# Kernel optimization log

Hardware: AMD Instinct MI355X
Metric: run time of the kernel (lower is better)

## Reference

```python
import jax, jax.numpy as jnp
import numpy as np
from jax import lax

C = 64
KS = 3  # filter_ks for dynamic kernel conv


def conv2d(x, w, pad, b=None):
    out = lax.conv_general_dilated(x, w, (1, 1), [(pad, pad), (pad, pad)],
                                   dimension_numbers=("NCHW", "OIHW", "NCHW"))
    if b is not None:
        out = out + b.reshape(1, -1, 1, 1)
    return out


def kernel_conv2d(feat, kernel):
    # feat: [B,C,H,W]; kernel: [B,C*KS*KS,H,W] -> per-pixel per-channel 3x3 filter
    B, Cc, H, W = feat.shape
    pad = (KS - 1) // 2
    xp = jnp.pad(feat, ((0, 0), (0, 0), (pad, pad), (pad, pad)), mode="edge")
    # patches: [B,C,KS*KS,H,W]
    patches = jnp.stack([xp[:, :, i:i + H, j:j + W]
                         for i in range(KS) for j in range(KS)], axis=2)
    K = kernel.reshape(B, Cc, KS * KS, H, W)
    return jnp.sum(patches * K, axis=2)


def setup_inputs() -> dict:
    key = jax.random.key(0)
    ks = jax.random.split(key, 24)
    B, H, W = 8, 128, 128
    s = lambda *sh: 1.0 / np.sqrt(np.prod(sh[1:]))
    def w(k, *sh):
        return jax.random.normal(k, sh, dtype=jnp.float32) * s(*sh)
    return {
        "f_event": jax.random.normal(ks[0], (B, C, H, W), dtype=jnp.float32),
        "f_blur": jax.random.normal(ks[1], (B, C, H, W), dtype=jnp.float32),
        # trans: conv3x3 -> ReLU -> conv3x3 (no bias)
        "Wt1": w(ks[2], C, C, 3, 3), "Wt2": w(ks[3], C, C, 3, 3),
        # trans2: conv3x3 -> ReLU
        "Wt3": w(ks[4], C, C, 3, 3),
        # F_mlp: Linear(C,2C) -> ReLU -> Linear(2C,C) -> Sigmoid
        "A1": w(ks[5], 2 * C, C), "b1": jnp.zeros((2 * C,), jnp.float32),
        "A2": w(ks[6], C, 2 * C), "b2": jnp.zeros((C,), jnp.float32),
        # gernerate_kernel: conv3x3(bias) -> ReLU -> conv1x1(bias) to C*KS^2
        "G1": w(ks[7], C, C, 3, 3), "g1b": jnp.zeros((C,), jnp.float32),
        "G2": w(ks[8], C * KS * KS, C, 1, 1), "g2b": jnp.zeros((C * KS * KS,), jnp.float32),
        # gate_rgb: conv1x1 C->1, bias
        "Rw": w(ks[9], 1, C, 1, 1), "rb": jnp.zeros((1,), jnp.float32),
        # body_sa: conv3x3 -> ReLU -> conv3x3 (no bias)
        "S1": w(ks[10], C, C, 3, 3), "S2": w(ks[11], C, C, 3, 3),
        # spatial_e: BasicConv(2,1,5,pad=2,relu=False), bias
        "Ew": w(ks[12], 1, 2, 5, 5), "eb": jnp.zeros((1,), jnp.float32),
        # conv1x1_fusion: 2C->2C, no bias
        "Fw": w(ks[13], 2 * C, 2 * C, 1, 1),
    }


def reference(f_event, f_blur, Wt1, Wt2, Wt3, A1, b1, A2, b2,
              G1, g1b, G2, g2b, Rw, rb, S1, S2, Ew, eb, Fw):
    fused = f_event + f_blur
    fused = conv2d(jax.nn.relu(conv2d(fused, Wt1, 1)), Wt2, 1)  # trans
    # SE-style channel gate
    w0 = jnp.mean(fused, axis=(2, 3))                      # [B,C]
    w0 = jax.nn.relu(w0 @ A1.T + b1)
    w0 = jax.nn.sigmoid(w0 @ A2.T + b2)                    # [B,C]
    f_b = f_blur + w0[:, :, None, None] * f_blur
    fused2 = fused + jax.nn.relu(conv2d(fused, Wt3, 1))    # trans2 + residual
    rgb_att = conv2d(fused2, Rw, 0, rb)                    # [B,1,H,W]
    f_b = f_b + rgb_att * f_b
    # dynamic per-pixel kernel from events
    kern = conv2d(jax.nn.relu(conv2d(f_event, G1, 1, g1b)), G2, 0, g2b)
    f_b = f_b + kernel_conv2d(f_b, kern)
    # spatial attention on events
    sa = conv2d(jax.nn.relu(conv2d(f_event, S1, 1)), S2, 1)
    comp = jnp.concatenate([jnp.max(sa, axis=1, keepdims=True),
                            jnp.mean(sa, axis=1, keepdims=True)], axis=1)
    scale_e = jax.nn.sigmoid(conv2d(comp, Ew, 2, eb))      # [B,1,H,W]
    f_e = f_event + scale_e * f_event
    res = conv2d(jnp.concatenate([f_e, f_b], axis=1), Fw, 0)
    return res
```

## Files before the change

kernel.cpp:

```cpp
#include <hip/hip_runtime.h>
#include <math.h>

constexpr int Bn = 8, Cn = 64, Hn = 128, Wn = 128;
constexpr int HW  = Hn * Wn;
constexpr int CHW = Cn * HW;
constexpr size_t NB = (size_t)Bn * CHW;

typedef float  f32x4  __attribute__((ext_vector_type(4)));
typedef __bf16 bf16x8 __attribute__((ext_vector_type(8)));
typedef unsigned int u32x4 __attribute__((ext_vector_type(4)));
typedef unsigned int u32x2 __attribute__((ext_vector_type(2)));

static __device__ __forceinline__ unsigned short f2bf(float f) {
    unsigned u = __builtin_bit_cast(unsigned, f);
    u = (u + 0x7FFF + ((u >> 16) & 1)) >> 16;
    return (unsigned short)u;
}
static __device__ __forceinline__ float bf2f(unsigned short v) {
    unsigned u = (unsigned)v << 16;
    return __builtin_bit_cast(float, u);
}
static __device__ __forceinline__ float bfhalf(unsigned u, int hi) {
    unsigned r = hi ? (u & 0xffff0000u) : (u << 16);
    return __builtin_bit_cast(float, r);
}

__global__ void prep_w_k(const float* __restrict__ W0, const float* __restrict__ W1,
                         const float* __restrict__ W2, const float* __restrict__ W3,
                         const float* __restrict__ W4, const float* __restrict__ W5,
                         unsigned short* __restrict__ dst) {
    int i = blockIdx.x * 256 + threadIdx.x;
    if (i >= 36864) return;
    const float* W = W0;
    switch (blockIdx.y) {
        case 1: W = W1; break; case 2: W = W2; break;
        case 3: W = W3; break; case 4: W = W4; break; case 5: W = W5; break;
        default: break;
    }
    int cj = i & 7;
    int rest = i >> 3;
    int co = rest & 63;
    rest >>= 6;
    int t  = rest % 9;
    int hs = rest / 9;
    int ci = hs * 8 + cj;
    dst[(size_t)blockIdx.y * 36864 + i] = f2bf(W[(co * 64 + ci) * 9 + t]);
}

__global__ void prep2_k(const float* __restrict__ G2, const float* __restrict__ Fw,
                        unsigned short* __restrict__ G2p, unsigned short* __restrict__ Fwp) {
    int i = blockIdx.x * 256 + threadIdx.x;
    if (i < 36864) G2p[i] = f2bf(G2[i]);
    else if (i < 36864 + 16384) Fwp[i - 36864] = f2bf(Fw[i - 36864]);
}

__global__ void pre_blk_k(const float* __restrict__ fe, const float* __restrict__ fb,
                          unsigned short* __restrict__ evb, unsigned short* __restrict__ f0b,
                          unsigned short* __restrict__ fbb) {
    int i = blockIdx.x * 256 + threadIdx.x;
    int px = i & 16383;
    int oct = (i >> 14) & 7;
    int b = i >> 17;
    const float* pe = fe + (size_t)b * CHW + (size_t)oct * 8 * HW + px;
    const float* pb = fb + (size_t)b * CHW + (size_t)oct * 8 * HW + px;
    u32x4 ev, f0, fbv;
#pragma unroll
    for (int q = 0; q < 4; ++q) {
        float e0 = pe[(size_t)(2 * q) * HW],     b0 = pb[(size_t)(2 * q) * HW];
        float e1 = pe[(size_t)(2 * q + 1) * HW], b1 = pb[(size_t)(2 * q + 1) * HW];
        ev[q]  = (unsigned)f2bf(e0) | ((unsigned)f2bf(e1) << 16);
        f0[q]  = (unsigned)f2bf(e0 + b0) | ((unsigned)f2bf(e1 + b1) << 16);
        fbv[q] = (unsigned)f2bf(b0) | ((unsigned)f2bf(b1) << 16);
    }
    const size_t o = ((size_t)(b * 8 + oct) * HW + px) * 8;
    *(u32x4*)(evb + o) = ev;
    *(u32x4*)(f0b + o) = f0;
    *(u32x4*)(fbb + o) = fbv;
}

template<bool RELU, bool BIAS, bool ADD_INPUT, bool RGB, bool COMP, bool STORE>
__global__ __launch_bounds__(256, 3) void conv3x3_blk(
        const unsigned short* __restrict__ in, const unsigned short* __restrict__ Wg,
        const float* __restrict__ bias, unsigned short* __restrict__ out,
        const float* __restrict__ gw, const float* __restrict__ gb,
        float* __restrict__ gout) {
    __shared__ unsigned short smIn[20736];
    const int b  = blockIdx.z;
    const int by = blockIdx.y << 4, bx = blockIdx.x << 4;
    const int tid = threadIdx.x;
    const int lane = tid & 63, w = tid >> 6;
    const int lx = lane & 15, ls = lane >> 4;

    for (int idx = tid; idx < 2592; idx += 256) {
        int oct = idx / 324;
        int p   = idx - oct * 324;
        int yy = p / 18, xx = p - yy * 18;
        int gy = by + yy - 1, gx = bx + xx - 1;
        u32x4 v = u32x4{0u, 0u, 0u, 0u};
        if ((unsigned)gy < (unsigned)Hn && (unsigned)gx < (unsigned)Wn)
            v = *(const u32x4*)(in + ((size_t)(b * 8 + oct) * HW + gy * Wn + gx) * 8);
        *(u32x4*)(smIn + idx * 8) = v;
    }
    __syncthreads();

    f32x4 acc[4][4];
#pragma unroll
    for (int m = 0; m < 4; ++m)
#pragma unroll
        for (int n = 0; n < 4; ++n) acc[m][n] = f32x4{0.f, 0.f, 0.f, 0.f};

#pragma unroll
    for (int ky = 0; ky < 3; ++ky)
#pragma unroll
    for (int kx = 0; kx < 3; ++kx) {
        const int t = ky * 3 + kx;
#pragma unroll
        for (int kk = 0; kk < 2; ++kk) {
            bf16x8 a[4];
            const unsigned short* wbase = Wg + kk * 18432 + ls * 4608 + t * 512 + lx * 8;
#pragma unroll
            for (int m = 0; m < 4; ++m)
                a[m] = *(const bf16x8*)(wbase + m * 128);
            const unsigned short* ibase =
                smIn + ((kk * 4 + ls) * 324 + (4 * w + ky) * 18 + lx + kx) * 8;
#pragma unroll
            for (int n = 0; n < 4; ++n) {
                bf16x8 bf = *(const bf16x8*)(ibase + n * 144);
#pragma unroll
                for (int m = 0; m < 4; ++m)
                    acc[m][n] = __builtin_amdgcn_mfma_f32_16x16x32_bf16(
                        a[m], bf, acc[m][n], 0, 0, 0);
            }
        }
    }

    const int y0 = by + 4 * w;
    float gs[4], gm[4];
    if constexpr (RGB || COMP) {
#pragma unroll
        for (int n = 0; n < 4; ++n) { gs[n] = 0.f; gm[n] = -1e30f; }
    }
#pragma unroll
    for (int m = 0; m < 4; ++m) {
        float4 rw4;
        if constexpr (RGB) rw4 = *(const float4*)(gw + 16 * m + ls * 4);
        const float rwf[4] = {RGB ? rw4.x : 0.f, RGB ? rw4.y : 0.f,
                              RGB ? rw4.z : 0.f, RGB ? rw4.w : 0.f};
        float bv[4] = {0.f, 0.f, 0.f, 0.f};
        if constexpr (BIAS) {
            float4 b4 = *(const float4*)(bias + 16 * m + ls * 4);
            bv[0] = b4.x; bv[1] = b4.y; bv[2] = b4.z; bv[3] = b4.w;
        }
        const size_t rowb = (size_t)(b * 8 + m * 2 + (ls >> 1)) * HW;
        const int j0 = (ls & 1) * 4;
#pragma unroll
        for (int n = 0; n < 4; ++n) {
            const size_t pofs = rowb + (size_t)(y0 + n) * Wn + bx + lx;
            u32x2 rin;
            if constexpr (ADD_INPUT) rin = *(const u32x2*)(in + pofs * 8 + j0);
            float vr[4];
#pragma unroll
            for (int r = 0; r < 4; ++r) {
                float v = acc[m][n][r] + bv[r];
                if constexpr (RELU) v = fmaxf(v, 0.f);
                if constexpr (ADD_INPUT) v += bfhalf(rin[r >> 1], r & 1);
                vr[r] = v;
                if constexpr (RGB) gs[n] = fmaf(rwf[r], v, gs[n]);
                if constexpr (COMP) { gm[n] = fmaxf(gm[n], v); gs[n] += v; }
            }
            if constexpr (STORE) {
                u32x2 pk;
                pk[0] = (unsigned)f2bf(vr[0]) | ((unsigned)f2bf(vr[1]) << 16);
                pk[1] = (unsigned)f2bf(vr[2]) | ((unsigned)f2bf(vr[3]) << 16);
                *(u32x2*)(out + pofs * 8 + j0) = pk;
            }
        }
    }
    if constexpr (RGB) {
#pragma unroll
        for (int n = 0; n < 4; ++n) {
            float s = gs[n];
            s += __shfl_xor(s, 16);
            s += __shfl_xor(s, 32);
            if (ls == 0)
                gout[(size_t)b * HW + (size_t)(y0 + n) * Wn + bx + lx] = s + gb[0];
        }
    }
    if constexpr (COMP) {
#pragma unroll
        for (int n = 0; n < 4; ++n) {
            float s = gs[n], mx = gm[n];
            s += __shfl_xor(s, 16);
            s += __shfl_xor(s, 32);
            mx = fmaxf(mx, __shfl_xor(mx, 16));
            mx = fmaxf(mx, __shfl_xor(mx, 32));
            if (ls == 0) {
                const size_t o = (size_t)b * 2 * HW + (size_t)(y0 + n) * Wn + bx + lx;
                gout[o]      = mx;
                gout[o + HW] = s * (1.f / 64.f);
            }
        }
    }
}

__global__ __launch_bounds__(256, 3) void conv3x3_dual_blk(
        const unsigned short* __restrict__ in, const unsigned short* __restrict__ W0,
        const unsigned short* __restrict__ W1, const float* __restrict__ bias0,
        unsigned short* __restrict__ out0, unsigned short* __restrict__ out1) {
    __shared__ unsigned short smIn[20736];
    const int z = blockIdx.z;
    const int b = z & 7, sel = z >> 3;
    const unsigned short* Wg = sel ? W1 : W0;
    unsigned short* out = sel ? out1 : out0;
    const int by = blockIdx.y << 4, bx = blockIdx.x << 4;
    const int tid = threadIdx.x;
    const int lane = tid & 63, w = tid >> 6;
    const int lx = lane & 15, ls = lane >> 4;

    for (int idx = tid; idx < 2592; idx += 256) {
        int oct = idx / 324;
        int p   = idx - oct * 324;
        int yy = p / 18, xx = p - yy * 18;
        int gy = by + yy - 1, gx = bx + xx - 1;
        u32x4 v = u32x4{0u, 0u, 0u, 0u};
        if ((unsigned)gy < (unsigned)Hn && (unsigned)gx < (unsigned)Wn)
            v = *(const u32x4*)(in + ((size_t)(b * 8 + oct) * HW + gy * Wn + gx) * 8);
        *(u32x4*)(smIn + idx * 8) = v;
    }
    __syncthreads();

    f32x4 acc[4][4];
#pragma unroll
    for (int m = 0; m < 4; ++m)
#pragma unroll
        for (int n = 0; n < 4; ++n) acc[m][n] = f32x4{0.f, 0.f, 0.f, 0.f};

#pragma unroll
    for (int ky = 0; ky < 3; ++ky)
#pragma unroll
    for (int kx = 0; kx < 3; ++kx) {
        const int t = ky * 3 + kx;
#pragma unroll
        for (int kk = 0; kk < 2; ++kk) {
            bf16x8 a[4];
            const unsigned short* wbase = Wg + kk * 18432 + ls * 4608 + t * 512 + lx * 8;
#pragma unroll
            for (int m = 0; m < 4; ++m)
                a[m] = *(const bf16x8*)(wbase + m * 128);
            const unsigned short* ibase =
                smIn + ((kk * 4 + ls) * 324 + (4 * w + ky) * 18 + lx + kx) * 8;
#pragma unroll
            for (int n = 0; n < 4; ++n) {
                bf16x8 bf = *(const bf16x8*)(ibase + n * 144);
#pragma unroll
                for (int m = 0; m < 4; ++m)
                    acc[m][n] = __builtin_amdgcn_mfma_f32_16x16x32_bf16(
                        a[m], bf, acc[m][n], 0, 0, 0);
            }
        }
    }

    const int y0 = by + 4 * w;
#pragma unroll
    for (int m = 0; m < 4; ++m) {
        float bv[4] = {0.f, 0.f, 0.f, 0.f};
        if (!sel) {
            float4 b4 = *(const float4*)(bias0 + 16 * m + ls * 4);
            bv[0] = b4.x; bv[1] = b4.y; bv[2] = b4.z; bv[3] = b4.w;
        }
        const size_t rowb = (size_t)(b * 8 + m * 2 + (ls >> 1)) * HW;
        const int j0 = (ls & 1) * 4;
#pragma unroll
        for (int n = 0; n < 4; ++n) {
            const size_t pofs = rowb + (size_t)(y0 + n) * Wn + bx + lx;
            float vr[4];
#pragma unroll
            for (int r = 0; r < 4; ++r)
                vr[r] = fmaxf(acc[m][n][r] + bv[r], 0.f);
            u32x2 pk;
            pk[0] = (unsigned)f2bf(vr[0]) | ((unsigned)f2bf(vr[1]) << 16);
            pk[1] = (unsigned)f2bf(vr[2]) | ((unsigned)f2bf(vr[3]) << 16);
            *(u32x2*)(out + pofs * 8 + j0) = pk;
        }
    }
}

__global__ void mean_hw_blk(const unsigned short* __restrict__ in, float* __restrict__ w0) {
    __shared__ float red[256][8];
    const int bo = blockIdx.x;
    const int tid = threadIdx.x;
    const unsigned short* p = in + (size_t)bo * HW * 8;
    float s[8];
#pragma unroll
    for (int j = 0; j < 8; ++j) s[j] = 0.f;
    for (int it = 0; it < 64; ++it) {
        u32x4 v = *(const u32x4*)(p + (size_t)(tid + it * 256) * 8);
#pragma unroll
        for (int j = 0; j < 8; ++j) s[j] += bfhalf(v[j >> 1], j & 1);
    }
#pragma unroll
    for (int j = 0; j < 8; ++j) red[tid][j] = s[j];
    __syncthreads();
    for (int off = 128; off > 0; off >>= 1) {
        if (tid < off)
#pragma unroll
            for (int j = 0; j < 8; ++j) red[tid][j] += red[tid + off][j];
        __syncthreads();
    }
    if (tid < 8) w0[bo * 8 + tid] = red[0][tid] * (1.f / 16384.f);
}

__global__ void mlp_k(const float* __restrict__ w0, const float* __restrict__ A1,
                      const float* __restrict__ b1, const float* __restrict__ A2,
                      const float* __restrict__ b2, float* __restrict__ w0s) {
    int b = blockIdx.x, t = threadIdx.x;
    __shared__ float w0r[64], hid[128];
    if (t < 64) w0r[t] = w0[b * 64 + t];
    __syncthreads();
    float s = b1[t];
    for (int c = 0; c < 64; ++c) s = fmaf(A1[t * 64 + c], w0r[c], s);
    hid[t] = fmaxf(s, 0.f);
    __syncthreads();
    if (t < 64) {
        float s2 = b2[t];
        for (int j = 0; j < 128; ++j) s2 = fmaf(A2[t * 128 + j], hid[j], s2);
        w0s[b * 64 + t] = 1.f / (1.f + expf(-s2));
    }
}

__global__ __launch_bounds__(256, 4) void dynfused_k(
        const unsigned short* __restrict__ fbb, const unsigned short* __restrict__ hb,
        const unsigned short* __restrict__ G2p, const float* __restrict__ g2b,
        const float* __restrict__ w0s, const float* __restrict__ rgb,
        unsigned short* __restrict__ outb) {
    __shared__ unsigned short smU[8192];
    __shared__ unsigned short smFB[11520];
    const int b  = blockIdx.z;
    const int by = blockIdx.y << 3, bx = blockIdx.x << 4;
    const int tid = threadIdx.x;
    const int lane = tid & 63, w = tid >> 6;
    const int lx = lane & 15, ls = lane >> 4;
    const int wr = w & 1, wc = w >> 1;
    const int px = tid & 127;
    const int chalf = __builtin_amdgcn_readfirstlane(tid >> 7);
    const int ty = px >> 4, tx = px & 15;

#pragma unroll
    for (int it = 0; it < 4; ++it) {
        int i = tid + it * 256;
        int p = i & 127, oct = i >> 7;
        const unsigned short* sp =
            hb + ((size_t)(b * 8 + oct) * HW + (by + (p >> 4)) * Wn + bx + (p & 15)) * 8;
        ((u32x4*)smU)[oct * 128 + p] = *(const u32x4*)sp;
    }
    const float* rgbb = rgb + (size_t)b * HW;
    for (int i = tid; i < 1440; i += 256) {
        int oct = i / 180, p = i - oct * 180;
        int pr = p / 18, pc = p - pr * 18;
        int gy = min(max(by + pr - 1, 0), Hn - 1);
        int gx = min(max(bx + pc - 1, 0), Wn - 1);
        u32x4 v = *(const u32x4*)(fbb + ((size_t)(b * 8 + oct) * HW + gy * Wn + gx) * 8);
        float g = 1.f + rgbb[gy * Wn + gx];
        float4 s0 = *(const float4*)(w0s + b * 64 + oct * 8);
        float4 s1 = *(const float4*)(w0s + b * 64 + oct * 8 + 4);
        const float sc[8] = {1.f + s0.x, 1.f + s0.y, 1.f + s0.z, 1.f + s0.w,
                             1.f + s1.x, 1.f + s1.y, 1.f + s1.z, 1.f + s1.w};
#pragma unroll
        for (int j = 0; j < 8; ++j)
            smFB[(oct * 8 + j) * 180 + p] = f2bf(bfhalf(v[j >> 1], j & 1) * sc[j] * g);
    }
    __syncthreads();

    bf16x8 bv[2][4];
#pragma unroll
    for (int kk = 0; kk < 2; ++kk)
#pragma unroll
        for (int n = 0; n < 4; ++n)
            bv[kk][n] = *(const bf16x8*)(smU + ((kk * 4 + ls) * 128 + wc * 64 + n * 16 + lx) * 8);
    __syncthreads();

    float acc[32];
#pragma unroll
    for (int s = 0; s < 32; ++s) acc[s] = 0.f;

#pragma unroll
    for (int chunk = 0; chunk < 9; ++chunk) {
        f32x4 ka[2][4];
#pragma unroll
        for (int m = 0; m < 2; ++m)
#pragma unroll
            for (int n = 0; n < 4; ++n) ka[m][n] = f32x4{0.f, 0.f, 0.f, 0.f};
#pragma unroll
        for (int kk = 0; kk < 2; ++kk) {
            bf16x8 a[2];
#pragma unroll
            for (int m = 0; m < 2; ++m)
                a[m] = *(const bf16x8*)(G2p +
                        (size_t)(chunk * 64 + wr * 32 + m * 16 + lx) * 64 + kk * 32 + ls * 8);
#pragma unroll
            for (int n = 0; n < 4; ++n)
#pragma unroll
                for (int m = 0; m < 2; ++m)
                    ka[m][n] = __builtin_amdgcn_mfma_f32_16x16x32_bf16(a[m], bv[kk][n], ka[m][n], 0, 0, 0);
        }
#pragma unroll
        for (int m = 0; m < 2; ++m) {
            const float4 bb4 = *(const float4*)(g2b + chunk * 64 + wr * 32 + m * 16 + ls * 4);
            const float bb[4] = {bb4.x, bb4.y, bb4.z, bb4.w};
            const int rl0 = wr * 32 + m * 16 + ls * 4;
            const int gr = rl0 >> 3, sub = rl0 & 7;
#pragma unroll
            for (int n = 0; n < 4; ++n) {
                const int pxl = wc * 64 + n * 16 + lx;
                u32x2 pk;
                pk[0] = (unsigned)f2bf(ka[m][n][0] + bb[0]) |
                        ((unsigned)f2bf(ka[m][n][1] + bb[1]) << 16);
                pk[1] = (unsigned)f2bf(ka[m][n][2] + bb[2]) |
                        ((unsigned)f2bf(ka[m][n][3] + bb[3]) << 16);
                *(u32x2*)(smU + pxl * 64 + ((gr ^ (pxl & 7)) << 3) + sub) = pk;
            }
        }
        __syncthreads();
        u32x4 kvr[8];
#pragma unroll
        for (int k = 0; k < 8; ++k)
            kvr[k] = *(const u32x4*)(smU + px * 64 + ((k ^ (px & 7)) << 3));
#pragma unroll
        for (int rl = 0; rl < 64; ++rl) {
            const int r = chunk * 64 + rl;
            const int c = r / 9, t = r - c * 9;
            const int s = c >> 1;
            if ((c & 1) == chalf) {
                float kv = bfhalf(kvr[rl >> 3][(rl & 7) >> 1], rl & 1);
                float pv = bf2f(smFB[c * 180 + (ty + t / 3) * 18 + tx + (t % 3)]);
                acc[s] = fmaf(kv, pv, acc[s]);
            }
        }
        __syncthreads();
    }

#pragma unroll
    for (int s = 0; s < 32; ++s) {
        const int c = 2 * s + chalf;
        float res = bf2f(smFB[c * 180 + (ty + 1) * 18 + (tx + 1)]);
        smU[c * 128 + px] = f2bf(acc[s] + res);
    }
    __syncthreads();
#pragma unroll
    for (int it = 0; it < 4; ++it) {
        int i = tid + it * 256;
        int p = i & 127, oct = i >> 7;
        u32x4 pk;
#pragma unroll
        for (int q = 0; q < 4; ++q)
            pk[q] = (unsigned)smU[(oct * 8 + 2 * q) * 128 + p] |
                    ((unsigned)smU[(oct * 8 + 2 * q + 1) * 128 + p] << 16);
        *(u32x4*)(outb + ((size_t)(b * 8 + oct) * HW + (by + (p >> 4)) * Wn + bx + (p & 15)) * 8) = pk;
    }
}

__global__ __launch_bounds__(256, 2) void fuse_mfma_k(
        const unsigned short* __restrict__ evb, const float* __restrict__ scale,
        const unsigned short* __restrict__ fb2b, const unsigned short* __restrict__ Fwp,
        float* __restrict__ out) {
    __shared__ unsigned short smF[16384];
    const int bid = blockIdx.x;
    const int b = bid >> 7, px0 = (bid & 127) << 7;
    const int tid = threadIdx.x;
    const int lane = tid & 63, w = tid >> 6;
    const int lx = lane & 15, ls = lane >> 4;
    const int wr = w & 1, wc = w >> 1;
    const float* sc = scale + b * HW + px0;

#pragma unroll
    for (int it = 0; it < 8; ++it) {
        int slot = tid + it * 256;
        int oct = slot >> 7, pxl = slot & 127;
        u32x4 v;
        if (oct < 8) {
            v = *(const u32x4*)(evb + ((size_t)(b * 8 + oct) * HW + px0 + pxl) * 8);
            float s = 1.f + sc[pxl];
#pragma unroll
            for (int q = 0; q < 4; ++q)
                v[q] = (unsigned)f2bf(bfhalf(v[q], 0) * s) |
                       ((unsigned)f2bf(bfhalf(v[q], 1) * s) << 16);
        } else {
            v = *(const u32x4*)(fb2b + ((size_t)(b * 8 + oct - 8) * HW + px0 + pxl) * 8);
        }
        ((u32x4*)smF)[oct * 128 + pxl] = v;
    }
    __syncthreads();

    f32x4 acc[4][4];
#pragma unroll
    for (int m = 0; m < 4; ++m)
#pragma unroll
        for (int n = 0; n < 4; ++n) acc[m][n] = f32x4{0.f, 0.f, 0.f, 0.f};

#pragma unroll
    for (int kk = 0; kk < 4; ++kk) {
        bf16x8 a[4];
#pragma unroll
        for (int m = 0; m < 4; ++m)
            a[m] = *(const bf16x8*)(Fwp + (size_t)(wr * 64 + m * 16 + lx) * 128 + kk * 32 + ls * 8);
#pragma unroll
        for (int n = 0; n < 4; ++n) {
            bf16x8 bv = *(const bf16x8*)(smF + ((kk * 4 + ls) * 128 + wc * 64 + n * 16 + lx) * 8);
#pragma unroll
            for (int m = 0; m < 4; ++m)
                acc[m][n] = __builtin_amdgcn_mfma_f32_16x16x32_bf16(a[m], bv, acc[m][n], 0, 0, 0);
        }
    }

    const size_t ob = (size_t)b * 2 * CHW + px0 + wc * 64;
#pragma unroll
    for (int m = 0; m < 4; ++m)
#pragma unroll
        for (int n = 0; n < 4; ++n)
#pragma unroll
            for (int j = 0; j < 4; ++j) {
                const int co = wr * 64 + m * 16 + ls * 4 + j;
                out[ob + (size_t)co * HW + n * 16 + lx] = acc[m][n][j];
            }
}

__global__ void sconv5_k(const float* __restrict__ comp, const float* __restrict__ Ew,
                         const float* __restrict__ eb, float* __restrict__ scale) {
    int id = blockIdx.x * 256 + threadIdx.x;
    int b = id >> 14, p = id & 16383;
    int y = p >> 7, x = p & 127;
    const float* cb = comp + (size_t)b * 2 * HW;
    float acc = eb[0];
#pragma unroll
    for (int ch = 0; ch < 2; ++ch)
#pragma unroll
        for (int ky = 0; ky < 5; ++ky) {
            int gy = y + ky - 2;
            if ((unsigned)gy >= (unsigned)Hn) continue;
#pragma unroll
            for (int kx = 0; kx < 5; ++kx) {
                int gx = x + kx - 2;
                if ((unsigned)gx >= (unsigned)Wn) continue;
                acc = fmaf(Ew[ch * 25 + ky * 5 + kx], cb[ch * HW + gy * Wn + gx], acc);
            }
        }
    scale[id] = 1.f / (1.f + expf(-acc));
}

extern "C" void kernel_launch(void* const* d_in, const int* in_sizes, int n_in,
                              void* d_out, int out_size, void* d_ws, size_t ws_size,
                              hipStream_t stream) {
    const float* f_event = (const float*)d_in[0];
    const float* f_blur  = (const float*)d_in[1];
    const float* Wt1 = (const float*)d_in[2];
    const float* Wt2 = (const float*)d_in[3];
    const float* Wt3 = (const float*)d_in[4];
    const float* A1  = (const float*)d_in[5];
    const float* b1  = (const float*)d_in[6];
    const float* A2  = (const float*)d_in[7];
    const float* b2  = (const float*)d_in[8];
    const float* G1  = (const float*)d_in[9];
    const float* g1b = (const float*)d_in[10];
    const float* G2  = (const float*)d_in[11];
    const float* g2b = (const float*)d_in[12];
    const float* Rw  = (const float*)d_in[13];
    const float* rb  = (const float*)d_in[14];
    const float* S1  = (const float*)d_in[15];
    const float* S2  = (const float*)d_in[16];
    const float* Ew  = (const float*)d_in[17];
    const float* eb  = (const float*)d_in[18];
    const float* Fw  = (const float*)d_in[19];
    float* out = (float*)d_out;

    float* ws    = (float*)d_ws;
    float* w0    = ws;
    float* w0s   = w0 + 512;
    float* rgb   = w0s + 512;
    float* comp  = rgb + Bn * HW;
    float* scale = comp + 2 * Bn * HW;
    unsigned short* wprep = (unsigned short*)(scale + Bn * HW);
    unsigned short* G2p = wprep + 6 * 36864;
    unsigned short* Fwp = G2p + 36864;
    unsigned short* B0 = Fwp + 16384;
    unsigned short* B1 = B0 + NB;
    unsigned short* B2 = B1 + NB;
    unsigned short* B3 = B2 + NB;
    unsigned short* B4 = B3 + NB;
    unsigned short* B5 = B4 + NB;

    dim3 cgrid(Wn / 16, Hn / 16, Bn);
    dim3 cgrid2(Wn / 16, Hn / 16, 2 * Bn);

    prep_w_k<<<dim3(144, 6), 256, 0, stream>>>(Wt1, Wt2, Wt3, G1, S1, S2, wprep);
    prep2_k<<<208, 256, 0, stream>>>(G2, Fw, G2p, Fwp);
    pre_blk_k<<<4096, 256, 0, stream>>>(f_event, f_blur, B0, B1, B5);
    conv3x3_blk<true, false, false, false, false, true><<<cgrid, 256, 0, stream>>>(
        B1, wprep + 0 * 36864, nullptr, B2, nullptr, nullptr, nullptr);
    conv3x3_blk<false, false, false, false, false, true><<<cgrid, 256, 0, stream>>>(
        B2, wprep + 1 * 36864, nullptr, B3, nullptr, nullptr, nullptr);
    mean_hw_blk<<<Bn * 8, 256, 0, stream>>>(B3, w0);
    mlp_k<<<Bn, 128, 0, stream>>>(w0, A1, b1, A2, b2, w0s);
    conv3x3_blk<true, false, true, true, false, false><<<cgrid, 256, 0, stream>>>(
        B3, wprep + 2 * 36864, nullptr, nullptr, Rw, rb, rgb);
    conv3x3_dual_blk<<<cgrid2, 256, 0, stream>>>(
        B0, wprep + 3 * 36864, wprep + 4 * 36864, g1b, B4, B1);
    dynfused_k<<<dim3(8, 16, Bn), 256, 0, stream>>>(B5, B4, G2p, g2b, w0s, rgb, B3);
    conv3x3_blk<false, false, false, false, true, false><<<cgrid, 256, 0, stream>>>(
        B1, wprep + 5 * 36864, nullptr, nullptr, nullptr, nullptr, comp);
    sconv5_k<<<Bn * HW / 256, 256, 0, stream>>>(comp, Ew, eb, scale);
    fuse_mfma_k<<<Bn * HW / 128, 256, 0, stream>>>(B0, scale, B3, Fwp, out);
}
```

Measured before the change: 233.9 us.

## Batch independent 3x3 conv layers into wider multi-branch launches

Groups the first-layer convolutions of the trans, kernel-generation and spatial-attention branches into a single launch with 24 z-slices. The second-layer trans and spatial-attention convs are likewise combined into one 16-slice launch. This cuts the number of 3x3 conv launches and gives each launch more blocks to fill the GPU's compute units, where the separate 8-batch launches left much of it idle. It costs an extra bf16 scratch buffer (B6), placed after B5, which requires the workspace to be large enough. The sconv5 launch is also moved earlier in the stream.

```diff
diff --git a/kernel.cpp b/kernel.cpp
--- a/kernel.cpp
+++ b/kernel.cpp
@@ -203,15 +203,18 @@
     }
 }
 
-__global__ __launch_bounds__(256, 3) void conv3x3_dual_blk(
-        const unsigned short* __restrict__ in, const unsigned short* __restrict__ W0,
-        const unsigned short* __restrict__ W1, const float* __restrict__ bias0,
-        unsigned short* __restrict__ out0, unsigned short* __restrict__ out1) {
+__global__ __launch_bounds__(256, 3) void conv3x3_l1_blk(
+        const unsigned short* __restrict__ f0, const unsigned short* __restrict__ ev,
+        const unsigned short* __restrict__ Wt1g, const unsigned short* __restrict__ G1g,
+        const unsigned short* __restrict__ S1g, const float* __restrict__ g1b,
+        unsigned short* __restrict__ out_t1, unsigned short* __restrict__ out_h,
+        unsigned short* __restrict__ out_s1) {
     __shared__ unsigned short smIn[20736];
     const int z = blockIdx.z;
     const int b = z & 7, sel = z >> 3;
-    const unsigned short* Wg = sel ? W1 : W0;
-    unsigned short* out = sel ? out1 : out0;
+    const unsigned short* in = (sel == 0) ? f0 : ev;
+    const unsigned short* Wg = (sel == 0) ? Wt1g : ((sel == 1) ? G1g : S1g);
+    unsigned short* out = (sel == 0) ? out_t1 : ((sel == 1) ? out_h : out_s1);
     const int by = blockIdx.y << 4, bx = blockIdx.x << 4;
     const int tid = threadIdx.x;
     const int lane = tid & 63, w = tid >> 6;
@@ -264,8 +267,8 @@
 #pragma unroll
     for (int m = 0; m < 4; ++m) {
         float bv[4] = {0.f, 0.f, 0.f, 0.f};
-        if (!sel) {
-            float4 b4 = *(const float4*)(bias0 + 16 * m + ls * 4);
+        if (sel == 1) {
+            float4 b4 = *(const float4*)(g1b + 16 * m + ls * 4);
             bv[0] = b4.x; bv[1] = b4.y; bv[2] = b4.z; bv[3] = b4.w;
         }
         const size_t rowb = (size_t)(b * 8 + m * 2 + (ls >> 1)) * HW;
@@ -281,6 +284,108 @@
             pk[0] = (unsigned)f2bf(vr[0]) | ((unsigned)f2bf(vr[1]) << 16);
             pk[1] = (unsigned)f2bf(vr[2]) | ((unsigned)f2bf(vr[3]) << 16);
             *(u32x2*)(out + pofs * 8 + j0) = pk;
+        }
+    }
+}
+
+__global__ __launch_bounds__(256, 3) void conv3x3_l2_blk(
+        const unsigned short* __restrict__ t1, const unsigned short* __restrict__ s1,
+        const unsigned short* __restrict__ Wt2g, const unsigned short* __restrict__ S2g,
+        unsigned short* __restrict__ out_f, float* __restrict__ comp) {
+    __shared__ unsigned short smIn[20736];
+    const int z = blockIdx.z;
+    const int b = z & 7, sel = z >> 3;
+    const unsigned short* in = (sel == 0) ? t1 : s1;
+    const unsigned short* Wg = (sel == 0) ? Wt2g : S2g;
+    const int by = blockIdx.y << 4, bx = blockIdx.x << 4;
+    const int tid = threadIdx.x;
+    const int lane = tid & 63, w = tid >> 6;
+    const int lx = lane & 15, ls = lane >> 4;
+
+    for (int idx = tid; idx < 2592; idx += 256) {
+        int oct = idx / 324;
+        int p   = idx - oct * 324;
+        int yy = p / 18, xx = p - yy * 18;
+        int gy = by + yy - 1, gx = bx + xx - 1;
+        u32x4 v = u32x4{0u, 0u, 0u, 0u};
+        if ((unsigned)gy < (unsigned)Hn && (unsigned)gx < (unsigned)Wn)
+            v = *(const u32x4*)(in + ((size_t)(b * 8 + oct) * HW + gy * Wn + gx) * 8);
+        *(u32x4*)(smIn + idx * 8) = v;
+    }
+    __syncthreads();
+
+    f32x4 acc[4][4];
+#pragma unroll
+    for (int m = 0; m < 4; ++m)
+#pragma unroll
+        for (int n = 0; n < 4; ++n) acc[m][n] = f32x4{0.f, 0.f, 0.f, 0.f};
+
+#pragma unroll
+    for (int ky = 0; ky < 3; ++ky)
+#pragma unroll
+    for (int kx = 0; kx < 3; ++kx) {
+        const int t = ky * 3 + kx;
+#pragma unroll
+        for (int kk = 0; kk < 2; ++kk) {
+            bf16x8 a[4];
+            const unsigned short* wbase = Wg + kk * 18432 + ls * 4608 + t * 512 + lx * 8;
+#pragma unroll
+            for (int m = 0; m < 4; ++m)
+                a[m] = *(const bf16x8*)(wbase + m * 128);
+            const unsigned short* ibase =
+                smIn + ((kk * 4 + ls) * 324 + (4 * w + ky) * 18 + lx + kx) * 8;
+#pragma unroll
+            for (int n = 0; n < 4; ++n) {
+                bf16x8 bf = *(const bf16x8*)(ibase + n * 144);
+#pragma unroll
+                for (int m = 0; m < 4; ++m)
+                    acc[m][n] = __builtin_amdgcn_mfma_f32_16x16x32_bf16(
+                        a[m], bf, acc[m][n], 0, 0, 0);
+            }
+        }
+    }
+
+    const int y0 = by + 4 * w;
+    if (sel == 0) {
+#pragma unroll
+        for (int m = 0; m < 4; ++m) {
+            const size_t rowb = (size_t)(b * 8 + m * 2 + (ls >> 1)) * HW;
+            const int j0 = (ls & 1) * 4;
+#pragma unroll
+            for (int n = 0; n < 4; ++n) {
+                const size_t pofs = rowb + (size_t)(y0 + n) * Wn + bx + lx;
+                u32x2 pk;
+                pk[0] = (unsigned)f2bf(acc[m][n][0]) | ((unsigned)f2bf(acc[m][n][1]) << 16);
+                pk[1] = (unsigned)f2bf(acc[m][n][2]) | ((unsigned)f2bf(acc[m][n][3]) << 16);
+                *(u32x2*)(out_f + pofs * 8 + j0) = pk;
+            }
+        }
+    } else {
+        float gs[4], gm[4];
+#pragma unroll
+        for (int n = 0; n < 4; ++n) { gs[n] = 0.f; gm[n] = -1e30f; }
+#pragma unroll
+        for (int m = 0; m < 4; ++m)
+#pragma unroll
+            for (int r = 0; r < 4; ++r)
+#pragma unroll
+                for (int n = 0; n < 4; ++n) {
+                    float v = acc[m][n][r];
+                    gm[n] = fmaxf(gm[n], v);
+                    gs[n] += v;
+                }
+#pragma unroll
+        for (int n = 0; n < 4; ++n) {
+            float s = gs[n], mx = gm[n];
+            s += __shfl_xor(s, 16);
+            s += __shfl_xor(s, 32);
+            mx = fmaxf(mx, __shfl_xor(mx, 16));
+            mx = fmaxf(mx, __shfl_xor(mx, 32));
+            if (ls == 0) {
+                const size_t o = (size_t)b * 2 * HW + (size_t)(y0 + n) * Wn + bx + lx;
+                comp[o]      = mx;
+                comp[o + HW] = s * (1.f / 64.f);
+            }
         }
     }
 }
@@ -587,26 +692,21 @@
     unsigned short* B3 = B2 + NB;
     unsigned short* B4 = B3 + NB;
     unsigned short* B5 = B4 + NB;
-
-    dim3 cgrid(Wn / 16, Hn / 16, Bn);
-    dim3 cgrid2(Wn / 16, Hn / 16, 2 * Bn);
+    unsigned short* B6 = B5 + NB;
 
     prep_w_k<<<dim3(144, 6), 256, 0, stream>>>(Wt1, Wt2, Wt3, G1, S1, S2, wprep);
     prep2_k<<<208, 256, 0, stream>>>(G2, Fw, G2p, Fwp);
     pre_blk_k<<<4096, 256, 0, stream>>>(f_event, f_blur, B0, B1, B5);
-    conv3x3_blk<true, false, false, false, false, true><<<cgrid, 256, 0, stream>>>(
-        B1, wprep + 0 * 36864, nullptr, B2, nullptr, nullptr, nullptr);
-    conv3x3_blk<false, false, false, false, false, true><<<cgrid, 256, 0, stream>>>(
-        B2, wprep + 1 * 36864, nullptr, B3, nullptr, nullptr, nullptr);
+    conv3x3_l1_blk<<<dim3(8, 8, 24), 256, 0, stream>>>(
+        B1, B0, wprep + 0 * 36864, wprep + 3 * 36864, wprep + 4 * 36864, g1b,
+        B2, B4, B6);
+    conv3x3_l2_blk<<<dim3(8, 8, 16), 256, 0, stream>>>(
+        B2, B6, wprep + 1 * 36864, wprep + 5 * 36864, B3, comp);
     mean_hw_blk<<<Bn * 8, 256, 0, stream>>>(B3, w0);
     mlp_k<<<Bn, 128, 0, stream>>>(w0, A1, b1, A2, b2, w0s);
-    conv3x3_blk<true, false, true, true, false, false><<<cgrid, 256, 0, stream>>>(
+    sconv5_k<<<Bn * HW / 256, 256, 0, stream>>>(comp, Ew, eb, scale);
+    conv3x3_blk<true, false, true, true, false, false><<<dim3(8, 8, Bn), 256, 0, stream>>>(
         B3, wprep + 2 * 36864, nullptr, nullptr, Rw, rb, rgb);
-    conv3x3_dual_blk<<<cgrid2, 256, 0, stream>>>(
-        B0, wprep + 3 * 36864, wprep + 4 * 36864, g1b, B4, B1);
     dynfused_k<<<dim3(8, 16, Bn), 256, 0, stream>>>(B5, B4, G2p, g2b, w0s, rgb, B3);
-    conv3x3_blk<false, false, false, false, true, false><<<cgrid, 256, 0, stream>>>(
-        B1, wprep + 5 * 36864, nullptr, nullptr, nullptr, nullptr, comp);
-    sconv5_k<<<Bn * HW / 256, 256, 0, stream>>>(comp, Ew, eb, scale);
     fuse_mfma_k<<<Bn * HW / 128, 256, 0, stream>>>(B0, scale, B3, Fwp, out);
 }
```

Result: faster. 222.3 us (-5.0%).
